# Kernel tuning notes

Measured on AMD Instinct MI355X. Metric: run time of the kernel, lower is better.

## Reference

```python
import jax, jax.numpy as jnp
import numpy as np

DIM = 768
NUM_HEADS = 12
HEAD_DIM = DIM // NUM_HEADS
SCALE = HEAD_DIM ** (-0.5)
LN_EPS = 1e-5


def setup_inputs() -> dict:
    key = jax.random.key(0)
    ks = jax.random.split(key, 8)
    B, K, C = 4, 2048, DIM
    return {
        "x": jax.random.normal(ks[0], (B, K, C), jnp.float32),
        "pos_embed": jax.random.normal(ks[1], (B, K, C), jnp.float32),
        "rel_pos_bias": jax.random.normal(ks[2], (B, K, K), jnp.float32),
        "ln_g": jnp.ones((C,), jnp.float32),
        "ln_b": jnp.zeros((C,), jnp.float32),
        "qkv_w": jax.random.normal(ks[3], (C, 3 * C), jnp.float32) * 0.02,
        "qkv_b": jnp.zeros((3 * C,), jnp.float32),
        "proj_w": jax.random.normal(ks[4], (C, C), jnp.float32) * 0.02,
        "proj_b": jnp.zeros((C,), jnp.float32),
    }


def _layernorm(x, g, b):
    mu = jnp.mean(x, axis=-1, keepdims=True)
    var = jnp.mean(jnp.square(x - mu), axis=-1, keepdims=True)
    return (x - mu) * jax.lax.rsqrt(var + LN_EPS) * g + b


def reference(x, pos_embed, rel_pos_bias, ln_g, ln_b, qkv_w, qkv_b, proj_w, proj_b):
    B, K, C = x.shape
    H, D = NUM_HEADS, HEAD_DIM
    xp = _layernorm(x, ln_g, ln_b) + pos_embed
    qkv = xp @ qkv_w + qkv_b                      # [B,K,3C]
    qkv = qkv.reshape(B, K, 3, H, D)
    q = jnp.transpose(qkv[:, :, 0], (0, 2, 1, 3))  # [B,H,K,D]
    k = jnp.transpose(qkv[:, :, 1], (0, 2, 1, 3))
    v = jnp.transpose(qkv[:, :, 2], (0, 2, 1, 3))
    attn = jnp.einsum("bhqd,bhkd->bhqk", q, k) * SCALE
    attn = attn + rel_pos_bias[:, None, :, :]
    attn = jax.nn.softmax(attn, axis=-1)
    out = jnp.einsum("bhqk,bhkd->bhqd", attn, v)   # [B,H,K,D]
    out = jnp.transpose(out, (0, 2, 1, 3)).reshape(B, K, C)
    # DropPath(0.1) is identity in eval mode
    return out @ proj_w + proj_b
```

## Files before the change

kernel.cpp:

```cpp
#include <hip/hip_runtime.h>
#include <hip/hip_bf16.h>
#include <stdint.h>

typedef __attribute__((ext_vector_type(4))) float f32x4;
typedef __attribute__((ext_vector_type(16))) float f32x16;
typedef __attribute__((ext_vector_type(8))) short s16x8;
typedef __attribute__((ext_vector_type(4))) short s16x4;
typedef uint16_t u16;

#define DEV __device__ __forceinline__

static DEV u16 f2bf(float f) {
  union { float f; uint32_t u; } v; v.f = f;
  uint32_t r = v.u + 0x7fffu + ((v.u >> 16) & 1u);
  return (u16)(r >> 16);
}

static DEV uint32_t cvt_pk_bf16(float lo, float hi) {
  uint32_t r;
  asm("v_cvt_pk_bf16_f32 %0, %1, %2" : "=v"(r) : "v"(lo), "v"(hi));
  return r;
}

#define GLD_LDS16(gp, lp) __builtin_amdgcn_global_load_lds( \
    (const __attribute__((address_space(1))) void*)(gp),    \
    (__attribute__((address_space(3))) void*)(lp), 16, 0, 0)

__global__ __launch_bounds__(256) void k_ln(
    const float* __restrict__ x, const float* __restrict__ pos,
    const float* __restrict__ g, const float* __restrict__ be,
    u16* __restrict__ xp) {
  int row = blockIdx.x;
  size_t base = (size_t)row * 768;
  int t = threadIdx.x;
  float v0 = x[base + t], v1 = x[base + t + 256], v2 = x[base + t + 512];
  float s = v0 + v1 + v2;
  float ss = v0 * v0 + v1 * v1 + v2 * v2;
#pragma unroll
  for (int off = 1; off < 64; off <<= 1) {
    s += __shfl_xor(s, off);
    ss += __shfl_xor(ss, off);
  }
  __shared__ float red[8];
  int wave = t >> 6, lane = t & 63;
  if (lane == 0) { red[wave] = s; red[4 + wave] = ss; }
  __syncthreads();
  float tot = red[0] + red[1] + red[2] + red[3];
  float tss = red[4] + red[5] + red[6] + red[7];
  float mu = tot * (1.0f / 768.0f);
  float var = tss * (1.0f / 768.0f) - mu * mu;
  float rs = rsqrtf(var + 1e-5f);
  float vv[3] = {v0, v1, v2};
#pragma unroll
  for (int i = 0; i < 3; ++i) {
    int c = t + i * 256;
    float val = (vv[i] - mu) * rs * g[c] + be[c] + pos[base + c];
    xp[base + c] = f2bf(val);
  }
}

__global__ __launch_bounds__(256) void k_tr(
    const float* __restrict__ in, u16* __restrict__ out, int K, int N) {
  __shared__ float tile[32][33];
  int n0 = blockIdx.x * 32, k0 = blockIdx.y * 32;
  int tx = threadIdx.x & 31, ty = threadIdx.x >> 5;
#pragma unroll
  for (int r = ty; r < 32; r += 8)
    tile[r][tx] = in[(size_t)(k0 + r) * N + n0 + tx];
  __syncthreads();
#pragma unroll
  for (int r = ty; r < 32; r += 8)
    out[(size_t)(n0 + r) * K + k0 + tx] = f2bf(tile[tx][r]);
}

__global__ __launch_bounds__(256) void k_gemm_qkv(
    const u16* __restrict__ A, const u16* __restrict__ Bt,
    const float* __restrict__ bias, u16* __restrict__ qkv,
    u16* __restrict__ vtg) {
  __shared__ u16 Al[128 * 64];
  __shared__ u16 Bl[128 * 64];
  const size_t BHKD = (size_t)48 * 2048 * 64;
  int mt = blockIdx.x, nt = blockIdx.y;
  int t = threadIdx.x, wave = t >> 6, lane = t & 63;
  int lr = lane & 15, lg = lane >> 4;
  f32x4 acc[4][4];
#pragma unroll
  for (int i = 0; i < 4; ++i)
#pragma unroll
    for (int j = 0; j < 4; ++j) acc[i][j] = (f32x4){0.f, 0.f, 0.f, 0.f};
  const size_t Ab = (size_t)mt * 128 * 768;
  const size_t Bb = (size_t)nt * 128 * 768;
  int wr = (wave >> 1) * 64, wc = (wave & 1) * 64;
  for (int kt = 0; kt < 12; ++kt) {
#pragma unroll
    for (int c = 0; c < 4; ++c) {
      int q = c * 256 + t;
      int row = q >> 3, ch = q & 7;
      int sc = ch ^ (row & 7);
      GLD_LDS16(A + Ab + (size_t)row * 768 + kt * 64 + sc * 8,
                &Al[(size_t)(c * 256 + wave * 64) * 8]);
      GLD_LDS16(Bt + Bb + (size_t)row * 768 + kt * 64 + sc * 8,
                &Bl[(size_t)(c * 256 + wave * 64) * 8]);
    }
    __syncthreads();
#pragma unroll
    for (int ki = 0; ki < 2; ++ki) {
      s16x8 af[4], bf[4];
#pragma unroll
      for (int mi = 0; mi < 4; ++mi)
        af[mi] = *(const s16x8*)&Al[(wr + mi * 16 + lr) * 64 +
                                    (((ki * 4 + lg) ^ (lr & 7)) * 8)];
#pragma unroll
      for (int ni = 0; ni < 4; ++ni)
        bf[ni] = *(const s16x8*)&Bl[(wc + ni * 16 + lr) * 64 +
                                    (((ki * 4 + lg) ^ (lr & 7)) * 8)];
#pragma unroll
      for (int mi = 0; mi < 4; ++mi)
#pragma unroll
        for (int ni = 0; ni < 4; ++ni)
          acc[mi][ni] = __builtin_amdgcn_mfma_f32_16x16x32_bf16(
              af[mi], bf[ni], acc[mi][ni], 0, 0, 0);
    }
    __syncthreads();
  }
#pragma unroll
  for (int ni = 0; ni < 4; ++ni) {
    int col = wc + ni * 16 + lr;
    int n = nt * 128 + col;
    int which = n / 768, cc = n % 768;
    int h = cc >> 6, d = cc & 63;
    float bs = bias[n];
    if (which == 2) {
#pragma unroll
      for (int mi = 0; mi < 4; ++mi) {
        int m0 = mt * 128 + wr + mi * 16 + lg * 4;
        int b = m0 >> 11, kp0 = m0 & 2047;
        s16x4 o4;
#pragma unroll
        for (int j = 0; j < 4; ++j) o4[j] = (short)f2bf(acc[mi][ni][j] + bs);
        *(s16x4*)&vtg[((size_t)(b * 12 + h) * 64 + d) * 2048 + kp0] = o4;
      }
    } else {
#pragma unroll
      for (int mi = 0; mi < 4; ++mi) {
#pragma unroll
        for (int j = 0; j < 4; ++j) {
          int row = wr + mi * 16 + lg * 4 + j;
          int m = mt * 128 + row;
          int b = m >> 11, kp = m & 2047;
          size_t dst = (size_t)which * BHKD +
                       (((size_t)b * 12 + h) * 2048 + kp) * 64 + d;
          qkv[dst] = f2bf(acc[mi][ni][j] + bs);
        }
      }
    }
  }
}

#define STAGE_KV(KB, VB, ktt) do {                                          \
  _Pragma("unroll")                                                         \
  for (int c_ = 0; c_ < 2; ++c_) {                                          \
    int q_ = c_ * 256 + t; int r_ = q_ >> 3, ch_ = q_ & 7;                  \
    int sc_ = ch_ ^ (r_ & 7);                                               \
    int gk_ = (r_ & 0x33) | ((r_ & 4) << 1) | ((r_ & 8) >> 1);              \
    GLD_LDS16(Kg + ((size_t)((ktt) * 64 + gk_)) * 64 + sc_ * 8,             \
              &KB[(c_ * 256 + wave * 64) * 8]);                             \
    GLD_LDS16(Vt + (size_t)r_ * 2048 + (ktt) * 64 + sc_ * 8,                \
              &VB[(c_ * 256 + wave * 64) * 8]);                             \
  }                                                                         \
} while (0)

#define LOAD_B(BR, ktt) do {                                                \
  _Pragma("unroll")                                                         \
  for (int kv_ = 0; kv_ < 2; ++kv_) {                                       \
    _Pragma("unroll")                                                       \
    for (int rn_ = 0; rn_ < 2; ++rn_) {                                     \
      const float* bp_ = Bgl + (ktt) * 64 + kv_ * 32 + rn_ * 16;            \
      BR[(kv_ * 2 + rn_) * 2]     = *(const f32x4*)bp_;                     \
      BR[(kv_ * 2 + rn_) * 2 + 1] = *(const f32x4*)(bp_ + 4);               \
    }                                                                       \
  }                                                                         \
} while (0)

#define COMPUTE_TILE(KB, VB, BV) do {                                       \
  f32x16 sa_[2];                                                            \
  _Pragma("unroll")                                                         \
  for (int r = 0; r < 16; ++r) { sa_[0][r] = 0.f; sa_[1][r] = 0.f; }        \
  _Pragma("unroll")                                                         \
  for (int ki = 0; ki < 4; ++ki) {                                          \
    _Pragma("unroll")                                                       \
    for (int kv_ = 0; kv_ < 2; ++kv_) {                                     \
      s16x8 kf = *(const s16x8*)&KB[(kv_ * 32 + l31) * 64 +                 \
                                    (((ki * 2 + hi) ^ (l31 & 7)) * 8)];     \
      sa_[kv_] = __builtin_amdgcn_mfma_f32_32x32x16_bf16(kf, qf[ki],        \
                                                         sa_[kv_], 0, 0, 0);\
    }                                                                       \
  }                                                                         \
  float p_[32];                                                             \
  _Pragma("unroll")                                                         \
  for (int kv_ = 0; kv_ < 2; ++kv_)                                         \
    _Pragma("unroll")                                                       \
    for (int r = 0; r < 16; ++r)                                            \
      p_[kv_ * 16 + r] = exp2f(                                             \
          __builtin_fmaf(sa_[kv_][r], 0.125f,                               \
              BV[kv_ * 4 + (r >> 3) * 2 + ((r >> 2) & 1)][r & 3]) *         \
          1.442695041f);                                                    \
  float tm_[16];                                                            \
  _Pragma("unroll")                                                         \
  for (int i = 0; i < 16; ++i) tm_[i] = p_[i] + p_[i + 16];                 \
  _Pragma("unroll")                                                         \
  for (int off = 8; off >= 1; off >>= 1)                                    \
    _Pragma("unroll")                                                       \
    for (int i = 0; i < off; ++i) tm_[i] += tm_[i + off];                   \
  l_run += tm_[0];                                                          \
  union { uint32_t u[4]; s16x8 v; } pa_[4];                                 \
  _Pragma("unroll")                                                         \
  for (int s = 0; s < 4; ++s)                                               \
    _Pragma("unroll")                                                       \
    for (int w = 0; w < 4; ++w)                                             \
      pa_[s].u[w] = cvt_pk_bf16(p_[(s >> 1) * 16 + (s & 1) * 8 + 2 * w],    \
                                p_[(s >> 1) * 16 + (s & 1) * 8 + 2 * w + 1]);\
  _Pragma("unroll")                                                         \
  for (int s = 0; s < 4; ++s) {                                             \
    _Pragma("unroll")                                                       \
    for (int dt = 0; dt < 2; ++dt) {                                        \
      s16x8 vf = *(const s16x8*)&VB[(dt * 32 + l31) * 64 +                  \
                                    (((s * 2 + hi) ^ (l31 & 7)) * 8)];      \
      oacc[dt] = __builtin_amdgcn_mfma_f32_32x32x16_bf16(vf, pa_[s].v,      \
                                                         oacc[dt], 0, 0, 0);\
    }                                                                       \
  }                                                                         \
} while (0)

__global__ __launch_bounds__(256, 3) void k_attn(
    const u16* __restrict__ qkv, const u16* __restrict__ vtg,
    const float* __restrict__ bias, u16* __restrict__ ctx) {
  __shared__ u16 Kl[3][64 * 64];
  __shared__ u16 Vl[3][64 * 64];
  int bid = blockIdx.x;
  int swz = (bid & 7) * 96 + (bid >> 3);
  int h = swz % 12;
  int bq = swz / 12;
  int qt = bq & 15;
  int b = bq >> 4;
  int bh = b * 12 + h;
  int t = threadIdx.x, wave = t >> 6, lane = t & 63;
  int l31 = lane & 31, hi = lane >> 5;
  const size_t BHKD = (size_t)48 * 2048 * 64;
  const u16* Q = qkv + (size_t)bh * 2048 * 64;
  const u16* Kg = Q + BHKD;
  const u16* Vt = vtg + (size_t)bh * 64 * 2048;
  int qrow = qt * 128 + wave * 32 + l31;
  const float* Bgl = bias + ((size_t)b * 2048 + qrow) * 2048 + hi * 8;
  s16x8 qf[4];
#pragma unroll
  for (int ki = 0; ki < 4; ++ki)
    qf[ki] = *(const s16x8*)&Q[(size_t)qrow * 64 + ki * 16 + hi * 8];
  f32x16 oacc[2];
#pragma unroll
  for (int r = 0; r < 16; ++r) { oacc[0][r] = 0.f; oacc[1][r] = 0.f; }
  float l_run = 0.f;

  STAGE_KV(Kl[0], Vl[0], 0);
  STAGE_KV(Kl[1], Vl[1], 1);
  asm volatile("s_waitcnt vmcnt(4)" ::: "memory");
  __builtin_amdgcn_s_barrier();
  __builtin_amdgcn_sched_barrier(0);

  int cur = 0;
#pragma unroll 1
  for (int kt = 0; kt < 32; ++kt) {
    f32x4 bv_[8];
    LOAD_B(bv_, kt);
    int nb = cur + 2; if (nb >= 3) nb -= 3;
    if (kt + 2 < 32) STAGE_KV(Kl[nb], Vl[nb], kt + 2);
    COMPUTE_TILE(Kl[cur], Vl[cur], bv_);
    asm volatile("s_waitcnt vmcnt(4)" ::: "memory");
    __builtin_amdgcn_sched_barrier(0);
    __builtin_amdgcn_s_barrier();
    __builtin_amdgcn_sched_barrier(0);
    cur = cur + 1; if (cur >= 3) cur = 0;
  }
  float l_tot = l_run + __shfl_xor(l_run, 32);
  float inv = 1.0f / l_tot;
  size_t obase = ((size_t)b * 2048 + qrow) * 768 + h * 64;
#pragma unroll
  for (int dt = 0; dt < 2; ++dt) {
#pragma unroll
    for (int g = 0; g < 4; ++g) {
      s16x4 o4;
#pragma unroll
      for (int j = 0; j < 4; ++j)
        o4[j] = (short)f2bf(oacc[dt][g * 4 + j] * inv);
      *(s16x4*)&ctx[obase + dt * 32 + g * 8 + hi * 4] = o4;
    }
  }
}

__global__ __launch_bounds__(256) void k_gemm_proj(
    const u16* __restrict__ A, const u16* __restrict__ Bt,
    const float* __restrict__ bias, float* __restrict__ out) {
  __shared__ u16 Al[128 * 64];
  __shared__ u16 Bl[128 * 64];
  int mt = blockIdx.x, nt = blockIdx.y;
  int t = threadIdx.x, wave = t >> 6, lane = t & 63;
  int lr = lane & 15, lg = lane >> 4;
  f32x4 acc[4][4];
#pragma unroll
  for (int i = 0; i < 4; ++i)
#pragma unroll
    for (int j = 0; j < 4; ++j) acc[i][j] = (f32x4){0.f, 0.f, 0.f, 0.f};
  const size_t Ab = (size_t)mt * 128 * 768;
  const size_t Bb = (size_t)nt * 128 * 768;
  int wr = (wave >> 1) * 64, wc = (wave & 1) * 64;
  for (int kt = 0; kt < 12; ++kt) {
#pragma unroll
    for (int c = 0; c < 4; ++c) {
      int q = c * 256 + t;
      int row = q >> 3, ch = q & 7;
      int sc = ch ^ (row & 7);
      GLD_LDS16(A + Ab + (size_t)row * 768 + kt * 64 + sc * 8,
                &Al[(size_t)(c * 256 + wave * 64) * 8]);
      GLD_LDS16(Bt + Bb + (size_t)row * 768 + kt * 64 + sc * 8,
                &Bl[(size_t)(c * 256 + wave * 64) * 8]);
    }
    __syncthreads();
#pragma unroll
    for (int ki = 0; ki < 2; ++ki) {
      s16x8 af[4], bf[4];
#pragma unroll
      for (int mi = 0; mi < 4; ++mi)
        af[mi] = *(const s16x8*)&Al[(wr + mi * 16 + lr) * 64 +
                                    (((ki * 4 + lg) ^ (lr & 7)) * 8)];
#pragma unroll
      for (int ni = 0; ni < 4; ++ni)
        bf[ni] = *(const s16x8*)&Bl[(wc + ni * 16 + lr) * 64 +
                                    (((ki * 4 + lg) ^ (lr & 7)) * 8)];
#pragma unroll
      for (int mi = 0; mi < 4; ++mi)
#pragma unroll
        for (int ni = 0; ni < 4; ++ni)
          acc[mi][ni] = __builtin_amdgcn_mfma_f32_16x16x32_bf16(
              af[mi], bf[ni], acc[mi][ni], 0, 0, 0);
    }
    __syncthreads();
  }
#pragma unroll
  for (int ni = 0; ni < 4; ++ni) {
    int col = wc + ni * 16 + lr;
    int n = nt * 128 + col;
    float bs = bias[n];
#pragma unroll
    for (int mi = 0; mi < 4; ++mi) {
#pragma unroll
      for (int j = 0; j < 4; ++j) {
        int row = wr + mi * 16 + lg * 4 + j;
        out[(size_t)(mt * 128 + row) * 768 + n] = acc[mi][ni][j] + bs;
      }
    }
  }
}

extern "C" void kernel_launch(void* const* d_in, const int* in_sizes, int n_in,
                              void* d_out, int out_size, void* d_ws, size_t ws_size,
                              hipStream_t stream) {
  const float* x      = (const float*)d_in[0];
  const float* pos    = (const float*)d_in[1];
  const float* bias   = (const float*)d_in[2];
  const float* ln_g   = (const float*)d_in[3];
  const float* ln_b   = (const float*)d_in[4];
  const float* qkv_w  = (const float*)d_in[5];
  const float* qkv_b  = (const float*)d_in[6];
  const float* proj_w = (const float*)d_in[7];
  const float* proj_b = (const float*)d_in[8];
  float* out = (float*)d_out;

  char* ws = (char*)d_ws;
  u16* xp      = (u16*)ws;              ws += 12582912;
  u16* qkv_wt  = (u16*)ws;              ws += 3538944;
  u16* proj_wt = (u16*)ws;              ws += 1179648;
  u16* qkvbuf  = (u16*)ws;              ws += 25165824;
  u16* ctx     = (u16*)ws;              ws += 12582912;
  u16* vtg     = (u16*)ws;              ws += 12582912;

  k_ln<<<8192, 256, 0, stream>>>(x, pos, ln_g, ln_b, xp);
  k_tr<<<dim3(72, 24), 256, 0, stream>>>(qkv_w, qkv_wt, 768, 2304);
  k_tr<<<dim3(24, 24), 256, 0, stream>>>(proj_w, proj_wt, 768, 768);
  k_gemm_qkv<<<dim3(64, 18), 256, 0, stream>>>(xp, qkv_wt, qkv_b, qkvbuf, vtg);
  k_attn<<<768, 256, 0, stream>>>(qkvbuf, vtg, bias, ctx);
  k_gemm_proj<<<dim3(64, 6), 256, 0, stream>>>(ctx, proj_wt, proj_b, out);
}
```

Measured before the change: 203.4 us.

## Fold softmax scale into Q, preload bias into MFMA accumulators, sum rows via MFMA

The QKV GEMM epilogue now multiplies Q by scale*log2(e), so the attention scores come out already in the exp2 domain. Each score accumulator is initialised with bias*log2(e) before the QK MFMAs, which removes the per-element FMA and multiply before exp2. The row-sum of probabilities is now computed by an extra MFMA against a vector of bf16 ones, replacing the VALU add-reduction tree and the cross-lane shuffle. This trades VALU work for extra MFMA cycles and 16 more accumulator registers, and the denominator is now summed from bf16-rounded probabilities.

```diff
diff --git a/kernel.cpp b/kernel.cpp
--- a/kernel.cpp
+++ b/kernel.cpp
@@ -123,6 +123,8 @@
     }
     __syncthreads();
   }
+  int which0 = (nt * 128) / 768;
+  float qscale = (which0 == 0) ? 0.1803368801f : 1.0f;
 #pragma unroll
   for (int ni = 0; ni < 4; ++ni) {
     int col = wc + ni * 16 + lr;
@@ -150,7 +152,7 @@
           int b = m >> 11, kp = m & 2047;
           size_t dst = (size_t)which * BHKD +
                        (((size_t)b * 12 + h) * 2048 + kp) * 64 + d;
-          qkv[dst] = f2bf(acc[mi][ni][j] + bs);
+          qkv[dst] = f2bf((acc[mi][ni][j] + bs) * qscale);
         }
       }
     }
@@ -185,7 +187,11 @@
 #define COMPUTE_TILE(KB, VB, BV) do {                                       \
   f32x16 sa_[2];                                                            \
   _Pragma("unroll")                                                         \
-  for (int r = 0; r < 16; ++r) { sa_[0][r] = 0.f; sa_[1][r] = 0.f; }        \
+  for (int kv_ = 0; kv_ < 2; ++kv_)                                         \
+    _Pragma("unroll")                                                       \
+    for (int r = 0; r < 16; ++r)                                            \
+      sa_[kv_][r] = 1.4426950409f *                                         \
+          BV[kv_ * 4 + (r >> 3) * 2 + ((r >> 2) & 1)][r & 3];               \
   _Pragma("unroll")                                                         \
   for (int ki = 0; ki < 4; ++ki) {                                          \
     _Pragma("unroll")                                                       \
@@ -201,18 +207,7 @@
   for (int kv_ = 0; kv_ < 2; ++kv_)                                         \
     _Pragma("unroll")                                                       \
     for (int r = 0; r < 16; ++r)                                            \
-      p_[kv_ * 16 + r] = exp2f(                                             \
-          __builtin_fmaf(sa_[kv_][r], 0.125f,                               \
-              BV[kv_ * 4 + (r >> 3) * 2 + ((r >> 2) & 1)][r & 3]) *         \
-          1.442695041f);                                                    \
-  float tm_[16];                                                            \
-  _Pragma("unroll")                                                         \
-  for (int i = 0; i < 16; ++i) tm_[i] = p_[i] + p_[i + 16];                 \
-  _Pragma("unroll")                                                         \
-  for (int off = 8; off >= 1; off >>= 1)                                    \
-    _Pragma("unroll")                                                       \
-    for (int i = 0; i < off; ++i) tm_[i] += tm_[i + off];                   \
-  l_run += tm_[0];                                                          \
+      p_[kv_ * 16 + r] = exp2f(sa_[kv_][r]);                                \
   union { uint32_t u[4]; s16x8 v; } pa_[4];                                 \
   _Pragma("unroll")                                                         \
   for (int s = 0; s < 4; ++s)                                               \
@@ -222,6 +217,8 @@
                                 p_[(s >> 1) * 16 + (s & 1) * 8 + 2 * w + 1]);\
   _Pragma("unroll")                                                         \
   for (int s = 0; s < 4; ++s) {                                             \
+    lacc = __builtin_amdgcn_mfma_f32_32x32x16_bf16(onesv, pa_[s].v,         \
+                                                   lacc, 0, 0, 0);          \
     _Pragma("unroll")                                                       \
     for (int dt = 0; dt < 2; ++dt) {                                        \
       s16x8 vf = *(const s16x8*)&VB[(dt * 32 + l31) * 64 +                  \
@@ -256,10 +253,12 @@
 #pragma unroll
   for (int ki = 0; ki < 4; ++ki)
     qf[ki] = *(const s16x8*)&Q[(size_t)qrow * 64 + ki * 16 + hi * 8];
-  f32x16 oacc[2];
-#pragma unroll
-  for (int r = 0; r < 16; ++r) { oacc[0][r] = 0.f; oacc[1][r] = 0.f; }
-  float l_run = 0.f;
+  s16x8 onesv;
+#pragma unroll
+  for (int i = 0; i < 8; ++i) onesv[i] = (short)0x3F80;
+  f32x16 oacc[2], lacc;
+#pragma unroll
+  for (int r = 0; r < 16; ++r) { oacc[0][r] = 0.f; oacc[1][r] = 0.f; lacc[r] = 0.f; }
 
   STAGE_KV(Kl[0], Vl[0], 0);
   STAGE_KV(Kl[1], Vl[1], 1);
@@ -281,8 +280,7 @@
     __builtin_amdgcn_sched_barrier(0);
     cur = cur + 1; if (cur >= 3) cur = 0;
   }
-  float l_tot = l_run + __shfl_xor(l_run, 32);
-  float inv = 1.0f / l_tot;
+  float inv = 1.0f / lacc[0];
   size_t obase = ((size_t)b * 2048 + qrow) * 768 + h * 64;
 #pragma unroll
   for (int dt = 0; dt < 2; ++dt) {
```

New measurement: 206.8 us. No clear change (+1.7%).

## Pre-convert bias to bf16 and fold softmax scale into Q and accumulator init

Applied to the files above, without the earlier changes.

Adds a pre-pass converting the relative-position bias to bf16, premultiplied by log2(e), which halves the bias bytes the attention kernel re-reads for every head. The softmax scale and log2(e) are folded into Q in the QKV GEMM epilogue. The QK MFMA accumulator is seeded with the bias, removing the per-element FMA before exp2. Wave priority is raised around MFMA blocks. The cost is an extra kernel pass and a workspace buffer, plus reduced precision of bias and Q.

```diff
diff --git a/kernel.cpp b/kernel.cpp
--- a/kernel.cpp
+++ b/kernel.cpp
@@ -16,6 +16,11 @@
   return (u16)(r >> 16);
 }
 
+static DEV float bf2f(u16 x) {
+  union { uint32_t u; float f; } v; v.u = ((uint32_t)x) << 16;
+  return v.f;
+}
+
 static DEV uint32_t cvt_pk_bf16(float lo, float hi) {
   uint32_t r;
   asm("v_cvt_pk_bf16_f32 %0, %1, %2" : "=v"(r) : "v"(lo), "v"(hi));
@@ -25,6 +30,19 @@
 #define GLD_LDS16(gp, lp) __builtin_amdgcn_global_load_lds( \
     (const __attribute__((address_space(1))) void*)(gp),    \
     (__attribute__((address_space(3))) void*)(lp), 16, 0, 0)
+
+__global__ __launch_bounds__(256) void k_bcast(
+    const float* __restrict__ in, u16* __restrict__ out) {
+  size_t i = ((size_t)blockIdx.x * 256 + threadIdx.x) * 8;
+  f32x4 a = *(const f32x4*)(in + i);
+  f32x4 b = *(const f32x4*)(in + i + 4);
+  s16x8 o;
+#pragma unroll
+  for (int j = 0; j < 4; ++j) o[j] = (short)f2bf(a[j] * 1.4426950409f);
+#pragma unroll
+  for (int j = 0; j < 4; ++j) o[4 + j] = (short)f2bf(b[j] * 1.4426950409f);
+  *(s16x8*)(out + i) = o;
+}
 
 __global__ __launch_bounds__(256) void k_ln(
     const float* __restrict__ x, const float* __restrict__ pos,
@@ -123,6 +141,8 @@
     }
     __syncthreads();
   }
+  int which0 = (nt * 128) / 768;
+  float qscale = (which0 == 0) ? 0.1803368801f : 1.0f;
 #pragma unroll
   for (int ni = 0; ni < 4; ++ni) {
     int col = wc + ni * 16 + lr;
@@ -150,7 +170,7 @@
           int b = m >> 11, kp = m & 2047;
           size_t dst = (size_t)which * BHKD +
                        (((size_t)b * 12 + h) * 2048 + kp) * 64 + d;
-          qkv[dst] = f2bf(acc[mi][ni][j] + bs);
+          qkv[dst] = f2bf((acc[mi][ni][j] + bs) * qscale);
         }
       }
     }
@@ -171,21 +191,21 @@
 } while (0)
 
 #define LOAD_B(BR, ktt) do {                                                \
-  _Pragma("unroll")                                                         \
-  for (int kv_ = 0; kv_ < 2; ++kv_) {                                       \
-    _Pragma("unroll")                                                       \
-    for (int rn_ = 0; rn_ < 2; ++rn_) {                                     \
-      const float* bp_ = Bgl + (ktt) * 64 + kv_ * 32 + rn_ * 16;            \
-      BR[(kv_ * 2 + rn_) * 2]     = *(const f32x4*)bp_;                     \
-      BR[(kv_ * 2 + rn_) * 2 + 1] = *(const f32x4*)(bp_ + 4);               \
-    }                                                                       \
-  }                                                                         \
+  const u16* bp_ = Bgl + (ktt) * 64;                                        \
+  BR[0] = *(const s16x8*)(bp_);                                             \
+  BR[1] = *(const s16x8*)(bp_ + 16);                                        \
+  BR[2] = *(const s16x8*)(bp_ + 32);                                        \
+  BR[3] = *(const s16x8*)(bp_ + 48);                                        \
 } while (0)
 
 #define COMPUTE_TILE(KB, VB, BV) do {                                       \
   f32x16 sa_[2];                                                            \
   _Pragma("unroll")                                                         \
-  for (int r = 0; r < 16; ++r) { sa_[0][r] = 0.f; sa_[1][r] = 0.f; }        \
+  for (int kv_ = 0; kv_ < 2; ++kv_)                                         \
+    _Pragma("unroll")                                                       \
+    for (int r = 0; r < 16; ++r)                                            \
+      sa_[kv_][r] = bf2f((u16)BV[kv_ * 2 + (r >> 3)][r & 7]);               \
+  __builtin_amdgcn_s_setprio(1);                                            \
   _Pragma("unroll")                                                         \
   for (int ki = 0; ki < 4; ++ki) {                                          \
     _Pragma("unroll")                                                       \
@@ -196,15 +216,13 @@
                                                          sa_[kv_], 0, 0, 0);\
     }                                                                       \
   }                                                                         \
+  __builtin_amdgcn_s_setprio(0);                                            \
   float p_[32];                                                             \
   _Pragma("unroll")                                                         \
   for (int kv_ = 0; kv_ < 2; ++kv_)                                         \
     _Pragma("unroll")                                                       \
     for (int r = 0; r < 16; ++r)                                            \
-      p_[kv_ * 16 + r] = exp2f(                                             \
-          __builtin_fmaf(sa_[kv_][r], 0.125f,                               \
-              BV[kv_ * 4 + (r >> 3) * 2 + ((r >> 2) & 1)][r & 3]) *         \
-          1.442695041f);                                                    \
+      p_[kv_ * 16 + r] = exp2f(sa_[kv_][r]);                                \
   float tm_[16];                                                            \
   _Pragma("unroll")                                                         \
   for (int i = 0; i < 16; ++i) tm_[i] = p_[i] + p_[i + 16];                 \
@@ -220,6 +238,7 @@
     for (int w = 0; w < 4; ++w)                                             \
       pa_[s].u[w] = cvt_pk_bf16(p_[(s >> 1) * 16 + (s & 1) * 8 + 2 * w],    \
                                 p_[(s >> 1) * 16 + (s & 1) * 8 + 2 * w + 1]);\
+  __builtin_amdgcn_s_setprio(1);                                            \
   _Pragma("unroll")                                                         \
   for (int s = 0; s < 4; ++s) {                                             \
     _Pragma("unroll")                                                       \
@@ -230,11 +249,12 @@
                                                          oacc[dt], 0, 0, 0);\
     }                                                                       \
   }                                                                         \
+  __builtin_amdgcn_s_setprio(0);                                            \
 } while (0)
 
 __global__ __launch_bounds__(256, 3) void k_attn(
     const u16* __restrict__ qkv, const u16* __restrict__ vtg,
-    const float* __restrict__ bias, u16* __restrict__ ctx) {
+    const u16* __restrict__ biasb, u16* __restrict__ ctx) {
   __shared__ u16 Kl[3][64 * 64];
   __shared__ u16 Vl[3][64 * 64];
   int bid = blockIdx.x;
@@ -251,7 +271,7 @@
   const u16* Kg = Q + BHKD;
   const u16* Vt = vtg + (size_t)bh * 64 * 2048;
   int qrow = qt * 128 + wave * 32 + l31;
-  const float* Bgl = bias + ((size_t)b * 2048 + qrow) * 2048 + hi * 8;
+  const u16* Bgl = biasb + ((size_t)b * 2048 + qrow) * 2048 + hi * 8;
   s16x8 qf[4];
 #pragma unroll
   for (int ki = 0; ki < 4; ++ki)
@@ -270,7 +290,7 @@
   int cur = 0;
 #pragma unroll 1
   for (int kt = 0; kt < 32; ++kt) {
-    f32x4 bv_[8];
+    s16x8 bv_[4];
     LOAD_B(bv_, kt);
     int nb = cur + 2; if (nb >= 3) nb -= 3;
     if (kt + 2 < 32) STAGE_KV(Kl[nb], Vl[nb], kt + 2);
@@ -382,11 +402,13 @@
   u16* qkvbuf  = (u16*)ws;              ws += 25165824;
   u16* ctx     = (u16*)ws;              ws += 12582912;
   u16* vtg     = (u16*)ws;              ws += 12582912;
-
+  u16* biasb   = (u16*)ws;              ws += 33554432;
+
+  k_bcast<<<8192, 256, 0, stream>>>(bias, biasb);
   k_ln<<<8192, 256, 0, stream>>>(x, pos, ln_g, ln_b, xp);
   k_tr<<<dim3(72, 24), 256, 0, stream>>>(qkv_w, qkv_wt, 768, 2304);
   k_tr<<<dim3(24, 24), 256, 0, stream>>>(proj_w, proj_wt, 768, 768);
   k_gemm_qkv<<<dim3(64, 18), 256, 0, stream>>>(xp, qkv_wt, qkv_b, qkvbuf, vtg);
-  k_attn<<<768, 256, 0, stream>>>(qkvbuf, vtg, bias, ctx);
+  k_attn<<<768, 256, 0, stream>>>(qkvbuf, vtg, biasb, ctx);
   k_gemm_proj<<<dim3(64, 6), 256, 0, stream>>>(ctx, proj_wt, proj_b, out);
 }
```

Result: no change. 200.8 us (-1.3%).
